# Performance work log

Hardware: AMD Instinct MI355X
Metric: run time of the kernel (lower is better)

## Reference

```python
import jax, jax.numpy as jnp
import numpy as np

LAMBDA_W = 1.0
NEG_INF = -1e10


def setup_inputs() -> dict:
    key = jax.random.key(0)
    k1, k2, k3 = jax.random.split(key, 3)
    B, L, D = 8, 2048, 256
    h_x = jax.random.normal(k1, (B, L, D), dtype=jnp.float32)
    h_y = jax.random.normal(k2, (B, L, D), dtype=jnp.float32)
    # masks: valid prefix of 3/4 length, padded tail of zeros (exercises masking)
    valid = (3 * L) // 4
    base = (jnp.arange(L) < valid).astype(jnp.float32)
    x_mask = jnp.broadcast_to(base, (B, L))
    y_mask = jnp.broadcast_to(base, (B, L))
    # biaffine weight (n_label=1, no biases), init_value scaling kept at O(1)
    W = jax.random.normal(k3, (D, D), dtype=jnp.float32) / jnp.sqrt(jnp.float32(D))
    return {"h_x": h_x, "h_y": h_y, "x_mask": x_mask, "y_mask": y_mask, "W": W}


def reference(h_x, h_y, x_mask, y_mask, W):
    # src = h_x [B,Ls,D], pred = h_y [B,Lp,D]
    src, pred = h_x, h_y
    src_mask, pred_mask = x_mask, y_mask

    # cost_mx[b,p,s] = ||src[b,s] - pred[b,p]||_2, via ||a||^2+||b||^2-2ab
    src_sq = jnp.sum(src * src, axis=-1)            # [B,Ls]
    pred_sq = jnp.sum(pred * pred, axis=-1)         # [B,Lp]
    cross = jnp.einsum('bpd,bsd->bps', pred, src)   # [B,Lp,Ls]
    cost_mx = jnp.sqrt(jnp.maximum(pred_sq[:, :, None] + src_sq[:, None, :] - 2.0 * cross, 0.0))

    # biaffine scores: pred W src^T  -> [B,Lp,Ls]
    tr_mx = jnp.einsum('bpd,de,bse->bps', pred, W, src)

    # cost_mask[b,p,s] = pred_mask[b,p]*src_mask[b,s]
    cost_mask = pred_mask[:, :, None] * src_mask[:, None, :]
    tr_mx = jnp.where(cost_mask == 0, NEG_INF, tr_mx)
    tr_prob = jax.nn.softmax(tr_mx, axis=-1)

    flow_cost = tr_prob * cost_mx                   # [B,Lp,Ls]

    nL1 = jnp.sum(pred_mask, axis=-1, keepdims=True)  # [B,1]
    nL2 = jnp.sum(src_mask, axis=-1, keepdims=True)   # [B,1]
    fc = jnp.sum(flow_cost, axis=(1, 2), keepdims=True)  # [B,1,1]
    fc = fc / (nL1 * nL2)   # broadcasts [B,1,1]/[B,1] -> [B,B,1], matches torch
    fc = jnp.mean(fc)
    return fc * LAMBDA_W
```

## Files before the change

kernel.cpp:

```cpp
#include <hip/hip_runtime.h>
#include <math.h>
#include <stdint.h>

#define B_ 8
#define L_ 2048
#define D_ 256
#define NEG_INF_V (-1e10f)
#define NSTRIP 32

typedef __bf16 bf16x8 __attribute__((ext_vector_type(8)));
typedef float f32x4 __attribute__((ext_vector_type(4)));

#define MFMA16(a, b, c) __builtin_amdgcn_mfma_f32_16x16x32_bf16((a), (b), (c), 0, 0, 0)


__global__ __launch_bounds__(256) void convert_kernel(
    const float* __restrict__ x, const float* __restrict__ W,
    __bf16* __restrict__ srcFM, __bf16* __restrict__ WFM,
    float* __restrict__ src_sq) {
    int tid = threadIdx.x;
    int blk = blockIdx.x;
    if (blk < 1024) {
        int g = blk;
        __shared__ __align__(16) __bf16 sFM[512 * 8];
        __shared__ float sSQ[16];
        int kb = (tid & 31) >> 2, qq = tid & 3;
        #pragma unroll
        for (int pass = 0; pass < 2; ++pass) {
            int m = pass * 8 + (tid >> 5);
            const float* p = x + ((size_t)g * 16 + m) * D_ + (tid & 31) * 8;
            float4 v0 = *(const float4*)p;
            float4 v1 = *(const float4*)(p + 4);
            float ss = v0.x * v0.x + v0.y * v0.y + v0.z * v0.z + v0.w * v0.w +
                       v1.x * v1.x + v1.y * v1.y + v1.z * v1.z + v1.w * v1.w;
            #pragma unroll
            for (int o = 16; o > 0; o >>= 1) ss += __shfl_xor(ss, o, 64);
            if ((tid & 31) == 0) sSQ[m] = ss;
            union { __bf16 o[8]; bf16x8 v; } cv;
            cv.o[0] = (__bf16)v0.x; cv.o[1] = (__bf16)v0.y;
            cv.o[2] = (__bf16)v0.z; cv.o[3] = (__bf16)v0.w;
            cv.o[4] = (__bf16)v1.x; cv.o[5] = (__bf16)v1.y;
            cv.o[6] = (__bf16)v1.z; cv.o[7] = (__bf16)v1.w;
            *(bf16x8*)(sFM + (m * 32 + kb * 4 + qq) * 8) = cv.v;
        }
        __syncthreads();
        int G0 = tid * 2;
        int kb0 = G0 >> 6, q0 = (G0 >> 4) & 3, m0 = G0 & 15;
        bf16x8 a = *(const bf16x8*)(sFM + (m0 * 32 + kb0 * 4 + q0) * 8);
        bf16x8 bgr = *(const bf16x8*)(sFM + ((m0 + 1) * 32 + kb0 * 4 + q0) * 8);
        *(bf16x8*)(srcFM + ((size_t)g * 512 + G0) * 8) = a;
        *(bf16x8*)(srcFM + ((size_t)g * 512 + G0 + 1) * 8) = bgr;
        if (tid < 16) src_sq[g * 16 + tid] = sSQ[tid];
    } else {
        int idx = (blk - 1024) * 256 + tid;
        int m = idx & 15, q = (idx >> 4) & 3, kb = (idx >> 6) & 7, gn = idx >> 9;
        union { __bf16 o[8]; bf16x8 v; } cv;
        #pragma unroll
        for (int j = 0; j < 8; ++j)
            cv.o[j] = (__bf16)W[(size_t)(kb * 32 + q * 8 + j) * D_ + gn * 16 + m];
        *(bf16x8*)(WFM + (size_t)idx * 8) = cv.v;
    }
}

__global__ __launch_bounds__(256, 4) void predconv_predw(
    const float* __restrict__ y, const __bf16* __restrict__ WFM,
    const float* __restrict__ pred_mask,
    __bf16* __restrict__ predFM, float* __restrict__ pred_sq,
    __bf16* __restrict__ pwFM) {
    __shared__ __align__(16) __bf16 sP[64 * 264];
    __shared__ int flag;
    int tid = threadIdx.x, lane = tid & 63, wid = tid >> 6;
    int id = blockIdx.x;
    int b = id & 7, t8 = id >> 3;
    int g1 = b * 32 + t8;
    size_t R0 = (size_t)g1 * 64;
    if (tid == 0) flag = 0;
    __syncthreads();
    if (tid < 64) { if (pred_mask[R0 + tid] != 0.f) atomicOr(&flag, 1); }

    int q = lane >> 4, m = lane & 15;
    float ss = 0.f;
    const float* yb = y + (R0 + wid * 16 + m) * D_ + q * 8;
    __bf16* pfb = predFM + (((size_t)(g1 * 4 + wid) * 8) * 64 + lane) * 8;
    #pragma unroll
    for (int kb = 0; kb < 8; ++kb) {
        float4 v0 = *(const float4*)(yb + kb * 32);
        float4 v1 = *(const float4*)(yb + kb * 32 + 4);
        ss += v0.x * v0.x + v0.y * v0.y + v0.z * v0.z + v0.w * v0.w +
              v1.x * v1.x + v1.y * v1.y + v1.z * v1.z + v1.w * v1.w;
        union { __bf16 o[8]; bf16x8 v; } cv;
        cv.o[0] = (__bf16)v0.x; cv.o[1] = (__bf16)v0.y;
        cv.o[2] = (__bf16)v0.z; cv.o[3] = (__bf16)v0.w;
        cv.o[4] = (__bf16)v1.x; cv.o[5] = (__bf16)v1.y;
        cv.o[6] = (__bf16)v1.z; cv.o[7] = (__bf16)v1.w;
        *(bf16x8*)(sP + ((wid * 8 + kb) * 64 + lane) * 8) = cv.v;
        *(bf16x8*)(pfb + (size_t)kb * 512) = cv.v;
    }
    ss += __shfl_xor(ss, 16, 64);
    ss += __shfl_xor(ss, 32, 64);
    if (q == 0) pred_sq[R0 + wid * 16 + m] = ss;
    __syncthreads();
    if (!flag) return;

    int wp = wid >> 1, wn = wid & 1;
    f32x4 acc[2][8] = {};
    const __bf16* bB = WFM + ((size_t)(wn * 8) * 8 * 64 + lane) * 8;
    #pragma unroll
    for (int kb = 0; kb < 8; ++kb) {
        bf16x8 fA[2];
        #pragma unroll
        for (int a = 0; a < 2; ++a)
            fA[a] = *(const bf16x8*)(sP + (((wp * 2 + a) * 8 + kb) * 64 + lane) * 8);
        #pragma unroll
        for (int h = 0; h < 2; ++h) {
            bf16x8 fB[4];
            #pragma unroll
            for (int t = 0; t < 4; ++t)
                fB[t] = *(const bf16x8*)(bB + ((size_t)((h * 4 + t) * 8 + kb) * 64) * 8);
            #pragma unroll
            for (int a = 0; a < 2; ++a)
                #pragma unroll
                for (int t = 0; t < 4; ++t)
                    acc[a][h * 4 + t] = MFMA16(fA[a], fB[t], acc[a][h * 4 + t]);
        }
    }
    int cn = lane & 15;
    #pragma unroll
    for (int h = 0; h < 2; ++h) {
        __syncthreads();
        if (wn == h) {
            #pragma unroll
            for (int a = 0; a < 2; ++a)
                #pragma unroll
                for (int t = 0; t < 8; ++t)
                    #pragma unroll
                    for (int r = 0; r < 4; ++r)
                        sP[(wp * 32 + a * 16 + q * 4 + r) * 136 + t * 16 + cn] =
                            (__bf16)acc[a][t][r];
        }
        __syncthreads();
        #pragma unroll
        for (int i = 0; i < 4; ++i) {
            int idx = i * 256 + tid;
            int G = idx >> 8, kbl = (idx >> 6) & 3, qq = (idx >> 4) & 3, mm = idx & 15;
            bf16x8 v = *(const bf16x8*)(sP + (G * 16 + mm) * 136 + kbl * 32 + qq * 8);
            *(bf16x8*)(pwFM +
                       (((size_t)(g1 * 4 + G) * 8 + h * 4 + kbl) * 64 + qq * 16 + mm) * 8) = v;
        }
    }
}

__global__ __launch_bounds__(256, 4) void fused_mfma(
    const __bf16* __restrict__ srcFM, const __bf16* __restrict__ predFM,
    const __bf16* __restrict__ pwFM,
    const float* __restrict__ src_mask, const float* __restrict__ pred_mask,
    const float* __restrict__ src_sq, const float* __restrict__ pred_sq,
    float* __restrict__ m_part, float* __restrict__ l_part,
    float* __restrict__ w_part, float* __restrict__ Sarr,
    unsigned int* __restrict__ counter) {
    __shared__ __align__(16) __bf16 sS[64 * 256];
    __shared__ float sPM[128], sPSQ[128], sSM[64], sSSQ[64];
    __shared__ int flg[4];
    int tid = threadIdx.x, lane = tid & 63, wid = tid >> 6;
    int id = blockIdx.x;
    int b = id & 7, px = (id >> 3) & 15, syb = id >> 7;
    int p0 = px * 128, s0 = syb * 64;

    if (id == 0) {
        if (tid == 0) *counter = 0u;
        if (tid < 24) Sarr[tid] = 0.f;
    }
    if (tid < 4) flg[tid] = 0;
    __syncthreads();
    if (tid < 128) {
        float v = pred_mask[b * L_ + p0 + tid];
        sPM[tid] = v;
        sPSQ[tid] = pred_sq[b * L_ + p0 + tid];
        atomicOr(&flg[(v != 0.f) ? 0 : 1], 1);
    } else if (tid < 192) {
        int t = tid - 128;
        float v = src_mask[b * L_ + s0 + t];
        sSM[t] = v;
        sSSQ[t] = src_sq[b * L_ + s0 + t];
        atomicOr(&flg[(v != 0.f) ? 2 : 3], 1);
    }
    {
        const __bf16* g = srcFM + ((size_t)(b * 128 + syb * 4)) * 4096;
        #pragma unroll
        for (int i = 0; i < 8; ++i) {
            size_t off = (size_t)i * 2048 + tid * 8;
            *(bf16x8*)(sS + off) = *(const bf16x8*)(g + off);
        }
    }
    __syncthreads();
    const bool anyVP = flg[0] != 0, anyIP = flg[1] != 0, anyVS = flg[2] != 0;
    const bool doT = anyVP && anyVS;
    const bool doG = anyVS || anyIP;
    if (!doG) {
        if (tid < 128) {
            size_t o = (size_t)syb * (B_ * L_) + b * L_ + p0 + tid;
            m_part[o] = NEG_INF_V; l_part[o] = 64.f; w_part[o] = 0.f;
        }
        return;
    }

    const __bf16* bP = predFM + ((size_t)(b * 128 + px * 8 + wid * 2)) * 4096 + lane * 8;
    const __bf16* bW = pwFM + ((size_t)(b * 128 + px * 8 + wid * 2)) * 4096 + lane * 8;
    const __bf16* bS = sS + lane * 8;

    f32x4 aG[2][4] = {};
    f32x4 aT[2][4] = {};
    if (doT) {
        #pragma unroll
        for (int kb = 0; kb < 8; ++kb) {
            bf16x8 fP[2], fW[2], fB[4];
            #pragma unroll
            for (int m = 0; m < 2; ++m) {
                fP[m] = *(const bf16x8*)(bP + (m * 8 + kb) * 512);
                fW[m] = *(const bf16x8*)(bW + (m * 8 + kb) * 512);
            }
            #pragma unroll
            for (int t = 0; t < 4; ++t)
                fB[t] = *(const bf16x8*)(bS + (t * 8 + kb) * 512);
            #pragma unroll
            for (int m = 0; m < 2; ++m)
                #pragma unroll
                for (int t = 0; t < 4; ++t) {
                    aG[m][t] = MFMA16(fP[m], fB[t], aG[m][t]);
                    aT[m][t] = MFMA16(fW[m], fB[t], aT[m][t]);
                }
        }
    } else {
        #pragma unroll
        for (int kb = 0; kb < 8; ++kb) {
            bf16x8 fP[2], fB[4];
            #pragma unroll
            for (int m = 0; m < 2; ++m)
                fP[m] = *(const bf16x8*)(bP + (m * 8 + kb) * 512);
            #pragma unroll
            for (int t = 0; t < 4; ++t)
                fB[t] = *(const bf16x8*)(bS + (t * 8 + kb) * 512);
            #pragma unroll
            for (int m = 0; m < 2; ++m)
                #pragma unroll
                for (int t = 0; t < 4; ++t)
                    aG[m][t] = MFMA16(fP[m], fB[t], aG[m][t]);
        }
    }

    int q = lane >> 4, cn = lane & 15;
    float smv[4], sqv[4];
    #pragma unroll
    for (int t = 0; t < 4; ++t) {
        smv[t] = sSM[t * 16 + cn];
        sqv[t] = sSSQ[t * 16 + cn];
    }
    #pragma unroll
    for (int m = 0; m < 2; ++m) {
        int rbase = wid * 32 + m * 16 + q * 4;
        #pragma unroll
        for (int r = 0; r < 4; ++r) {
            float pm = sPM[rbase + r], psq = sPSQ[rbase + r];
            float tv[4], cst[4];
            float tm = -1e30f;
            #pragma unroll
            for (int t = 0; t < 4; ++t) {
                cst[t] = __builtin_amdgcn_sqrtf(
                    fmaxf(psq + sqv[t] - 2.f * aG[m][t][r], 0.f));
                float tt = doT ? aT[m][t][r] : NEG_INF_V;
                tv[t] = (pm == 0.f) ? 0.f : (smv[t] != 0.f ? tt : NEG_INF_V);
                tm = fmaxf(tm, tv[t]);
            }
            #pragma unroll
            for (int o = 8; o > 0; o >>= 1) tm = fmaxf(tm, __shfl_xor(tm, o, 16));
            float l = 0.f, w = 0.f;
            #pragma unroll
            for (int t = 0; t < 4; ++t) {
                float e = __expf(tv[t] - tm);
                l += e;
                w = fmaf(e, cst[t], w);
            }
            #pragma unroll
            for (int o = 8; o > 0; o >>= 1) {
                l += __shfl_xor(l, o, 16);
                w += __shfl_xor(w, o, 16);
            }
            if (cn == 0) {
                size_t o = (size_t)syb * (B_ * L_) + b * L_ + p0 + rbase + r;
                m_part[o] = tm;
                l_part[o] = l;
                w_part[o] = w;
            }
        }
    }
}

__global__ __launch_bounds__(256) void combine_kernel(
    const float* __restrict__ m_part, const float* __restrict__ l_part,
    const float* __restrict__ w_part,
    const float* __restrict__ x_mask, const float* __restrict__ y_mask,
    float* __restrict__ Sarr, unsigned int* __restrict__ counter,
    float* __restrict__ out) {
    int tid = threadIdx.x;
    int r = blockIdx.x * 256 + tid;
    int b = r >> 11;
    float mm = -1e30f;
    #pragma unroll
    for (int s = 0; s < NSTRIP; ++s) mm = fmaxf(mm, m_part[(size_t)s * (B_ * L_) + r]);
    float l = 0.f, w = 0.f;
    #pragma unroll
    for (int s = 0; s < NSTRIP; ++s) {
        size_t o = (size_t)s * (B_ * L_) + r;
        float e = __expf(m_part[o] - mm);
        l = fmaf(l_part[o], e, l);
        w = fmaf(w_part[o], e, w);
    }
    float sv = w / l;
    float n1 = y_mask[r], n2 = x_mask[r];
    __shared__ float red[3][256];
    red[0][tid] = sv; red[1][tid] = n1; red[2][tid] = n2;
    __syncthreads();
    for (int o = 128; o > 0; o >>= 1) {
        if (tid < o) {
            red[0][tid] += red[0][tid + o];
            red[1][tid] += red[1][tid + o];
            red[2][tid] += red[2][tid + o];
        }
        __syncthreads();
    }
    __shared__ int isLast;
    if (tid == 0) {
        atomicAdd(&Sarr[b], red[0][0]);
        atomicAdd(&Sarr[8 + b], red[1][0]);
        atomicAdd(&Sarr[16 + b], red[2][0]);
        __threadfence();
        isLast = (atomicAdd(counter, 1u) == 63u) ? 1 : 0;
    }
    __syncthreads();
    if (isLast) {
        __shared__ float fb[24];
        if (tid < 24) fb[tid] = atomicAdd(&Sarr[tid], 0.f);
        __syncthreads();
        if (tid == 0) {
            float ss = 0.f, si = 0.f;
            for (int bb = 0; bb < B_; bb++) {
                ss += fb[bb];
                si += 1.0f / (fb[8 + bb] * fb[16 + bb]);
            }
            out[0] = ss * si / (float)(B_ * B_);
        }
    }
}

extern "C" void kernel_launch(void* const* d_in, const int* in_sizes, int n_in,
                              void* d_out, int out_size, void* d_ws, size_t ws_size,
                              hipStream_t stream) {
    const float* h_x = (const float*)d_in[0];
    const float* h_y = (const float*)d_in[1];
    const float* x_mask = (const float*)d_in[2];
    const float* y_mask = (const float*)d_in[3];
    const float* W = (const float*)d_in[4];

    char* w8 = (char*)d_ws;
    const size_t BLD2 = (size_t)B_ * L_ * D_ * 2;
    __bf16* srcFM = (__bf16*)w8;
    __bf16* predFM = (__bf16*)(w8 + BLD2);
    __bf16* pwFM = (__bf16*)(w8 + 2 * BLD2);
    __bf16* WFM = (__bf16*)(w8 + 3 * BLD2);
    float* src_sq = (float*)(w8 + 3 * BLD2 + (1 << 17));
    float* pred_sq = (float*)(w8 + 3 * BLD2 + (1 << 17) + (1 << 16));
    char* pbase = w8 + 3 * BLD2 + (1 << 17) + (1 << 17);
    const size_t PSZ = (size_t)B_ * L_ * NSTRIP * 4;
    float* m_part = (float*)pbase;
    float* l_part = (float*)(pbase + PSZ);
    float* w_part = (float*)(pbase + 2 * PSZ);
    float* Sarr = (float*)(pbase + 3 * PSZ);
    unsigned int* counter = (unsigned int*)(pbase + 3 * PSZ + 128);

    convert_kernel<<<1056, 256, 0, stream>>>(h_x, W, srcFM, WFM, src_sq);
    predconv_predw<<<256, 256, 0, stream>>>(h_y, WFM, y_mask, predFM, pred_sq,
                                            pwFM);
    fused_mfma<<<4096, 256, 0, stream>>>(
        srcFM, predFM, pwFM, x_mask, y_mask, src_sq, pred_sq,
        m_part, l_part, w_part, Sarr, counter);
    combine_kernel<<<B_ * L_ / 256, 256, 0, stream>>>(
        m_part, l_part, w_part, x_mask, y_mask, Sarr, counter, (float*)d_out);
}
```

Baseline: 139.6 us.

## Replace split-strip partials and combine kernel with flash-style online softmax loop

The main kernel now has each block own 32 pred rows and loop over all 16 source tiles of 128 columns, keeping a running max, sum and weighted cost in registers. This removes the large m/l/w partial arrays and the separate combine kernel, and the pred/predW fragments stay in registers for the whole loop. Fully masked source tiles are skipped after the first valid one. The grid shrinks from 4096 to 512 blocks with double-size shared tiles and launch bounds of 2 blocks per CU, so occupancy and parallelism drop and each tile iteration is serialized by a syncthreads-guarded LDS reload.

```diff
diff --git a/kernel.cpp b/kernel.cpp
--- a/kernel.cpp
+++ b/kernel.cpp
@@ -6,7 +6,6 @@
 #define L_ 2048
 #define D_ 256
 #define NEG_INF_V (-1e10f)
-#define NSTRIP 32
 
 typedef __bf16 bf16x8 __attribute__((ext_vector_type(8)));
 typedef float f32x4 __attribute__((ext_vector_type(4)));
@@ -17,7 +16,8 @@
 __global__ __launch_bounds__(256) void convert_kernel(
     const float* __restrict__ x, const float* __restrict__ W,
     __bf16* __restrict__ srcFM, __bf16* __restrict__ WFM,
-    float* __restrict__ src_sq) {
+    float* __restrict__ src_sq,
+    float* __restrict__ Sarr, unsigned int* __restrict__ counter) {
     int tid = threadIdx.x;
     int blk = blockIdx.x;
     if (blk < 1024) {
@@ -52,6 +52,10 @@
         *(bf16x8*)(srcFM + ((size_t)g * 512 + G0 + 1) * 8) = bgr;
         if (tid < 16) src_sq[g * 16 + tid] = sSQ[tid];
     } else {
+        if (blk == 1024) {
+            if (tid < 24) Sarr[tid] = 0.f;
+            if (tid == 24) *counter = 0u;
+        }
         int idx = (blk - 1024) * 256 + tid;
         int m = idx & 15, q = (idx >> 4) & 3, kb = (idx >> 6) & 7, gn = idx >> 9;
         union { __bf16 o[8]; bf16x8 v; } cv;
@@ -150,191 +154,197 @@
     }
 }
 
-__global__ __launch_bounds__(256, 4) void fused_mfma(
+__global__ __launch_bounds__(256, 2) void flash_fused(
     const __bf16* __restrict__ srcFM, const __bf16* __restrict__ predFM,
     const __bf16* __restrict__ pwFM,
-    const float* __restrict__ src_mask, const float* __restrict__ pred_mask,
+    const float* __restrict__ x_mask, const float* __restrict__ y_mask,
     const float* __restrict__ src_sq, const float* __restrict__ pred_sq,
-    float* __restrict__ m_part, float* __restrict__ l_part,
-    float* __restrict__ w_part, float* __restrict__ Sarr,
-    unsigned int* __restrict__ counter) {
-    __shared__ __align__(16) __bf16 sS[64 * 256];
-    __shared__ float sPM[128], sPSQ[128], sSM[64], sSSQ[64];
-    __shared__ int flg[4];
+    float* __restrict__ Sarr, unsigned int* __restrict__ counter,
+    float* __restrict__ out) {
+    __shared__ __align__(16) __bf16 sS[2 * 64 * 256];
+    __shared__ float sSM2[128], sSSQ2[128];
+    __shared__ float sPM[32], sPSQ[32];
+    __shared__ int flgI[34];
+    __shared__ int isLast;
     int tid = threadIdx.x, lane = tid & 63, wid = tid >> 6;
-    int id = blockIdx.x;
-    int b = id & 7, px = (id >> 3) & 15, syb = id >> 7;
-    int p0 = px * 128, s0 = syb * 64;
-
-    if (id == 0) {
-        if (tid == 0) *counter = 0u;
-        if (tid < 24) Sarr[tid] = 0.f;
-    }
-    if (tid < 4) flg[tid] = 0;
-    __syncthreads();
-    if (tid < 128) {
-        float v = pred_mask[b * L_ + p0 + tid];
+    int rg = wid >> 1, sp = wid & 1;
+    int blk = blockIdx.x;
+    int b = blk & 7, pg = blk >> 3;
+    int p0 = pg * 32;
+
+    if (tid < 34) flgI[tid] = 0;
+    __syncthreads();
+    if (tid < 32) {
+        float v = y_mask[b * L_ + p0 + tid];
         sPM[tid] = v;
         sPSQ[tid] = pred_sq[b * L_ + p0 + tid];
-        atomicOr(&flg[(v != 0.f) ? 0 : 1], 1);
-    } else if (tid < 192) {
-        int t = tid - 128;
-        float v = src_mask[b * L_ + s0 + t];
-        sSM[t] = v;
-        sSSQ[t] = src_sq[b * L_ + s0 + t];
-        atomicOr(&flg[(v != 0.f) ? 2 : 3], 1);
+        atomicOr(&flgI[(v != 0.f) ? 32 : 33], 1);
     }
     {
-        const __bf16* g = srcFM + ((size_t)(b * 128 + syb * 4)) * 4096;
-        #pragma unroll
-        for (int i = 0; i < 8; ++i) {
-            size_t off = (size_t)i * 2048 + tid * 8;
-            *(bf16x8*)(sS + off) = *(const bf16x8*)(g + off);
-        }
-    }
-    __syncthreads();
-    const bool anyVP = flg[0] != 0, anyIP = flg[1] != 0, anyVS = flg[2] != 0;
-    const bool doT = anyVP && anyVS;
-    const bool doG = anyVS || anyIP;
-    if (!doG) {
-        if (tid < 128) {
-            size_t o = (size_t)syb * (B_ * L_) + b * L_ + p0 + tid;
-            m_part[o] = NEG_INF_V; l_part[o] = 64.f; w_part[o] = 0.f;
-        }
-        return;
-    }
-
-    const __bf16* bP = predFM + ((size_t)(b * 128 + px * 8 + wid * 2)) * 4096 + lane * 8;
-    const __bf16* bW = pwFM + ((size_t)(b * 128 + px * 8 + wid * 2)) * 4096 + lane * 8;
-    const __bf16* bS = sS + lane * 8;
-
-    f32x4 aG[2][4] = {};
-    f32x4 aT[2][4] = {};
-    if (doT) {
+        const float* xm = x_mask + b * L_;
+        int s0 = tid * 8;
+        int any = 0;
+        #pragma unroll
+        for (int j = 0; j < 8; ++j) any |= (xm[s0 + j] != 0.f) ? 1 : 0;
+        if (any) atomicOr(&flgI[s0 >> 6], 1);
+    }
+    __syncthreads();
+    unsigned int vmask = 0;
+    for (int s = 0; s < 32; ++s) vmask |= (flgI[s] ? 1u : 0u) << s;
+    const bool anyVP = flgI[32] != 0, anyIP = flgI[33] != 0;
+
+    int Gp = b * 128 + pg * 2 + rg;
+    bf16x8 fP[8], fW[8];
+    {
+        const __bf16* bP = predFM + (size_t)Gp * 4096 + lane * 8;
+        const __bf16* bW = pwFM + (size_t)Gp * 4096 + lane * 8;
         #pragma unroll
         for (int kb = 0; kb < 8; ++kb) {
-            bf16x8 fP[2], fW[2], fB[4];
-            #pragma unroll
-            for (int m = 0; m < 2; ++m) {
-                fP[m] = *(const bf16x8*)(bP + (m * 8 + kb) * 512);
-                fW[m] = *(const bf16x8*)(bW + (m * 8 + kb) * 512);
-            }
-            #pragma unroll
-            for (int t = 0; t < 4; ++t)
-                fB[t] = *(const bf16x8*)(bS + (t * 8 + kb) * 512);
-            #pragma unroll
-            for (int m = 0; m < 2; ++m)
-                #pragma unroll
-                for (int t = 0; t < 4; ++t) {
-                    aG[m][t] = MFMA16(fP[m], fB[t], aG[m][t]);
-                    aT[m][t] = MFMA16(fW[m], fB[t], aT[m][t]);
+            fP[kb] = *(const bf16x8*)(bP + kb * 512);
+            fW[kb] = *(const bf16x8*)(bW + kb * 512);
+        }
+    }
+    int q = lane >> 4, cn = lane & 15;
+    float pm4[4], psq4[4];
+    #pragma unroll
+    for (int r = 0; r < 4; ++r) {
+        pm4[r] = sPM[rg * 16 + q * 4 + r];
+        psq4[r] = sPSQ[rg * 16 + q * 4 + r];
+    }
+    float m4[4] = {-1e30f, -1e30f, -1e30f, -1e30f};
+    float l4[4] = {0.f, 0.f, 0.f, 0.f};
+    float w4[4] = {0.f, 0.f, 0.f, 0.f};
+
+    bool seen = false;
+    for (int t = 0; t < 16; ++t) {
+        bool v0 = (vmask >> (2 * t)) & 1, v1 = (vmask >> (2 * t + 1)) & 1;
+        if (!v0 && !v1 && !anyIP && seen) continue;
+        {
+            const __bf16* g = srcFM + ((size_t)(b * 128 + t * 8)) * 4096;
+            #pragma unroll
+            for (int i = 0; i < 16; ++i) {
+                size_t off = (size_t)i * 2048 + tid * 8;
+                *(bf16x8*)(sS + off) = *(const bf16x8*)(g + off);
+            }
+            if (tid < 128) {
+                int ssp = tid >> 6, si = tid & 63;
+                int sidx = b * L_ + (2 * t + ssp) * 64 + si;
+                sSM2[tid] = x_mask[sidx];
+                sSSQ2[tid] = src_sq[sidx];
+            }
+        }
+        __syncthreads();
+        bool vs = sp ? v1 : v0;
+        bool doTw = anyVP && vs;
+        const __bf16* bS = sS + sp * 16384 + lane * 8;
+        f32x4 aG[4] = {};
+        f32x4 aT[4] = {};
+        if (doTw) {
+            #pragma unroll
+            for (int kb = 0; kb < 8; ++kb) {
+                bf16x8 fB[4];
+                #pragma unroll
+                for (int ct = 0; ct < 4; ++ct)
+                    fB[ct] = *(const bf16x8*)(bS + (ct * 8 + kb) * 512);
+                #pragma unroll
+                for (int ct = 0; ct < 4; ++ct) {
+                    aG[ct] = MFMA16(fP[kb], fB[ct], aG[ct]);
+                    aT[ct] = MFMA16(fW[kb], fB[ct], aT[ct]);
                 }
-        }
-    } else {
-        #pragma unroll
-        for (int kb = 0; kb < 8; ++kb) {
-            bf16x8 fP[2], fB[4];
-            #pragma unroll
-            for (int m = 0; m < 2; ++m)
-                fP[m] = *(const bf16x8*)(bP + (m * 8 + kb) * 512);
-            #pragma unroll
-            for (int t = 0; t < 4; ++t)
-                fB[t] = *(const bf16x8*)(bS + (t * 8 + kb) * 512);
-            #pragma unroll
-            for (int m = 0; m < 2; ++m)
-                #pragma unroll
-                for (int t = 0; t < 4; ++t)
-                    aG[m][t] = MFMA16(fP[m], fB[t], aG[m][t]);
-        }
-    }
-
-    int q = lane >> 4, cn = lane & 15;
-    float smv[4], sqv[4];
-    #pragma unroll
-    for (int t = 0; t < 4; ++t) {
-        smv[t] = sSM[t * 16 + cn];
-        sqv[t] = sSSQ[t * 16 + cn];
-    }
-    #pragma unroll
-    for (int m = 0; m < 2; ++m) {
-        int rbase = wid * 32 + m * 16 + q * 4;
+            }
+        } else {
+            #pragma unroll
+            for (int kb = 0; kb < 8; ++kb) {
+                bf16x8 fB[4];
+                #pragma unroll
+                for (int ct = 0; ct < 4; ++ct)
+                    fB[ct] = *(const bf16x8*)(bS + (ct * 8 + kb) * 512);
+                #pragma unroll
+                for (int ct = 0; ct < 4; ++ct)
+                    aG[ct] = MFMA16(fP[kb], fB[ct], aG[ct]);
+            }
+        }
+        float smv[4], sqv[4];
+        #pragma unroll
+        for (int ct = 0; ct < 4; ++ct) {
+            smv[ct] = sSM2[sp * 64 + ct * 16 + cn];
+            sqv[ct] = sSSQ2[sp * 64 + ct * 16 + cn];
+        }
         #pragma unroll
         for (int r = 0; r < 4; ++r) {
-            float pm = sPM[rbase + r], psq = sPSQ[rbase + r];
+            float pm = pm4[r], psq = psq4[r];
             float tv[4], cst[4];
             float tm = -1e30f;
             #pragma unroll
-            for (int t = 0; t < 4; ++t) {
-                cst[t] = __builtin_amdgcn_sqrtf(
-                    fmaxf(psq + sqv[t] - 2.f * aG[m][t][r], 0.f));
-                float tt = doT ? aT[m][t][r] : NEG_INF_V;
-                tv[t] = (pm == 0.f) ? 0.f : (smv[t] != 0.f ? tt : NEG_INF_V);
-                tm = fmaxf(tm, tv[t]);
+            for (int ct = 0; ct < 4; ++ct) {
+                cst[ct] = __builtin_amdgcn_sqrtf(
+                    fmaxf(psq + sqv[ct] - 2.f * aG[ct][r], 0.f));
+                float tt = doTw ? aT[ct][r] : NEG_INF_V;
+                tv[ct] = (pm == 0.f) ? 0.f : (smv[ct] != 0.f ? tt : NEG_INF_V);
+                tm = fmaxf(tm, tv[ct]);
             }
             #pragma unroll
             for (int o = 8; o > 0; o >>= 1) tm = fmaxf(tm, __shfl_xor(tm, o, 16));
-            float l = 0.f, w = 0.f;
-            #pragma unroll
-            for (int t = 0; t < 4; ++t) {
-                float e = __expf(tv[t] - tm);
-                l += e;
-                w = fmaf(e, cst[t], w);
+            float le = 0.f, we = 0.f;
+            #pragma unroll
+            for (int ct = 0; ct < 4; ++ct) {
+                float e = __expf(tv[ct] - tm);
+                le += e;
+                we = fmaf(e, cst[ct], we);
             }
             #pragma unroll
             for (int o = 8; o > 0; o >>= 1) {
-                l += __shfl_xor(l, o, 16);
-                w += __shfl_xor(w, o, 16);
-            }
-            if (cn == 0) {
-                size_t o = (size_t)syb * (B_ * L_) + b * L_ + p0 + rbase + r;
-                m_part[o] = tm;
-                l_part[o] = l;
-                w_part[o] = w;
-            }
-        }
-    }
-}
-
-__global__ __launch_bounds__(256) void combine_kernel(
-    const float* __restrict__ m_part, const float* __restrict__ l_part,
-    const float* __restrict__ w_part,
-    const float* __restrict__ x_mask, const float* __restrict__ y_mask,
-    float* __restrict__ Sarr, unsigned int* __restrict__ counter,
-    float* __restrict__ out) {
-    int tid = threadIdx.x;
-    int r = blockIdx.x * 256 + tid;
-    int b = r >> 11;
-    float mm = -1e30f;
-    #pragma unroll
-    for (int s = 0; s < NSTRIP; ++s) mm = fmaxf(mm, m_part[(size_t)s * (B_ * L_) + r]);
-    float l = 0.f, w = 0.f;
-    #pragma unroll
-    for (int s = 0; s < NSTRIP; ++s) {
-        size_t o = (size_t)s * (B_ * L_) + r;
-        float e = __expf(m_part[o] - mm);
-        l = fmaf(l_part[o], e, l);
-        w = fmaf(w_part[o], e, w);
-    }
-    float sv = w / l;
-    float n1 = y_mask[r], n2 = x_mask[r];
-    __shared__ float red[3][256];
-    red[0][tid] = sv; red[1][tid] = n1; red[2][tid] = n2;
-    __syncthreads();
-    for (int o = 128; o > 0; o >>= 1) {
-        if (tid < o) {
-            red[0][tid] += red[0][tid + o];
-            red[1][tid] += red[1][tid + o];
-            red[2][tid] += red[2][tid + o];
-        }
-        __syncthreads();
-    }
-    __shared__ int isLast;
+                le += __shfl_xor(le, o, 16);
+                we += __shfl_xor(we, o, 16);
+            }
+            float M = fmaxf(m4[r], tm);
+            float e1 = __expf(m4[r] - M), e2 = __expf(tm - M);
+            l4[r] = l4[r] * e1 + le * e2;
+            w4[r] = w4[r] * e1 + we * e2;
+            m4[r] = M;
+        }
+        seen = seen || v0 || v1;
+        __syncthreads();
+    }
+
+    __syncthreads();
+    float* mrg = (float*)sS;
+    if (cn == 0) {
+        #pragma unroll
+        for (int r = 0; r < 4; ++r) {
+            int row = wid * 16 + q * 4 + r;
+            mrg[row * 3 + 0] = m4[r];
+            mrg[row * 3 + 1] = l4[r];
+            mrg[row * 3 + 2] = w4[r];
+        }
+    }
+    __syncthreads();
+    float sv = 0.f, n1 = 0.f, n2 = 0.f;
+    if (tid < 32) {
+        int rgi = tid >> 4, rr = tid & 15;
+        int rowA = (rgi * 2 + 0) * 16 + rr, rowB = (rgi * 2 + 1) * 16 + rr;
+        float ma = mrg[rowA * 3], la = mrg[rowA * 3 + 1], wa = mrg[rowA * 3 + 2];
+        float mb = mrg[rowB * 3], lb = mrg[rowB * 3 + 1], wb = mrg[rowB * 3 + 2];
+        float M = fmaxf(ma, mb);
+        float e1 = __expf(ma - M), e2 = __expf(mb - M);
+        float l = la * e1 + lb * e2;
+        float w = wa * e1 + wb * e2;
+        sv = w / l;
+        n1 = y_mask[b * L_ + p0 + tid];
+        n2 = x_mask[b * L_ + p0 + tid];
+    }
+    #pragma unroll
+    for (int o = 16; o > 0; o >>= 1) {
+        sv += __shfl_xor(sv, o, 32);
+        n1 += __shfl_xor(n1, o, 32);
+        n2 += __shfl_xor(n2, o, 32);
+    }
     if (tid == 0) {
-        atomicAdd(&Sarr[b], red[0][0]);
-        atomicAdd(&Sarr[8 + b], red[1][0]);
-        atomicAdd(&Sarr[16 + b], red[2][0]);
+        atomicAdd(&Sarr[b], sv);
+        atomicAdd(&Sarr[8 + b], n1);
+        atomicAdd(&Sarr[16 + b], n2);
         __threadfence();
-        isLast = (atomicAdd(counter, 1u) == 63u) ? 1 : 0;
+        isLast = (atomicAdd(counter, 1u) == 511u) ? 1 : 0;
     }
     __syncthreads();
     if (isLast) {
@@ -369,20 +379,15 @@
     __bf16* WFM = (__bf16*)(w8 + 3 * BLD2);
     float* src_sq = (float*)(w8 + 3 * BLD2 + (1 << 17));
     float* pred_sq = (float*)(w8 + 3 * BLD2 + (1 << 17) + (1 << 16));
-    char* pbase = w8 + 3 * BLD2 + (1 << 17) + (1 << 17);
-    const size_t PSZ = (size_t)B_ * L_ * NSTRIP * 4;
-    float* m_part = (float*)pbase;
-    float* l_part = (float*)(pbase + PSZ);
-    float* w_part = (float*)(pbase + 2 * PSZ);
-    float* Sarr = (float*)(pbase + 3 * PSZ);
-    unsigned int* counter = (unsigned int*)(pbase + 3 * PSZ + 128);
-
-    convert_kernel<<<1056, 256, 0, stream>>>(h_x, W, srcFM, WFM, src_sq);
+    char* ctrl = w8 + 3 * BLD2 + (1 << 17) + (1 << 17);
+    float* Sarr = (float*)ctrl;
+    unsigned int* counter = (unsigned int*)(ctrl + 128);
+
+    convert_kernel<<<1056, 256, 0, stream>>>(h_x, W, srcFM, WFM, src_sq,
+                                             Sarr, counter);
     predconv_predw<<<256, 256, 0, stream>>>(h_y, WFM, y_mask, predFM, pred_sq,
                                             pwFM);
-    fused_mfma<<<4096, 256, 0, stream>>>(
+    flash_fused<<<512, 256, 0, stream>>>(
         srcFM, predFM, pwFM, x_mask, y_mask, src_sq, pred_sq,
-        m_part, l_part, w_part, Sarr, counter);
-    combine_kernel<<<B_ * L_ / 256, 256, 0, stream>>>(
-        m_part, l_part, w_part, x_mask, y_mask, Sarr, counter, (float*)d_out);
+        Sarr, counter, (float*)d_out);
 }
```

Result: slower. 162.8 us (+16.6%).
